# Optimization experiments

Hardware: AMD Instinct MI355X
Metric: run time of the kernel (lower is better)

Reference implementation:

```python
import jax, jax.numpy as jnp
import numpy as np

B, H, S, DK, DV = 2, 16, 2048, 128, 128


def setup_inputs() -> dict:
    key = jax.random.key(0)
    kq, kk, kv = jax.random.split(key, 3)
    query = jax.random.normal(kq, (B, H, S, DK), dtype=jnp.float32)
    k_ = jax.random.normal(kk, (B, H, S, DK), dtype=jnp.float32)
    value = jax.random.normal(kv, (B, H, S, DV), dtype=jnp.float32)
    # causal mask: True = masked out (upper triangle above diagonal)
    causal = ~jnp.tril(jnp.ones((S, S), dtype=bool))
    mask = jnp.broadcast_to(causal[None, None, :, :], (B, 1, S, S))
    return {"query": query, "key": k_, "value": value, "mask": mask}


def reference(query, key, value, mask):
    d_k = query.shape[-1]
    # scores: (B, H, Sq, Sk)
    scores = jnp.einsum("bhqd,bhkd->bhqk", query, key) / jnp.sqrt(jnp.float32(d_k))
    scores = jnp.where(mask, -jnp.inf, scores)
    attention_weights = jax.nn.softmax(scores, axis=-1)
    # dropout p=0.0 (eval) -> identity
    output = jnp.einsum("bhqk,bhkv->bhqv", attention_weights, value)
    return (output, attention_weights)
```

## Files before the change

kernel.cpp:

```cpp
#include <hip/hip_runtime.h>
#include <hip/hip_bf16.h>


typedef __attribute__((ext_vector_type(4))) float  f32x4;
typedef __attribute__((ext_vector_type(8))) short  short8;
typedef __attribute__((ext_vector_type(4))) short  short4v;

#define S_LEN 2048
#define DKK   128
#define QBLK  64
#define KBLK  64
#define NBH   32

__device__ __forceinline__ short f2bf(float f) {
    return __builtin_bit_cast(short, __float2bfloat16(f));
}

__device__ __forceinline__ void g2l16(const void* g, void* l) {
    __builtin_amdgcn_global_load_lds(
        (const __attribute__((address_space(1))) unsigned int*)g,
        (__attribute__((address_space(3))) unsigned int*)l, 16, 0, 0);
}


__global__ __launch_bounds__(256) void conv_k(const float* __restrict__ K,
                                              short* __restrict__ Kb) {
    const int NCH = NBH * S_LEN * (DKK / 8);
    for (int g = blockIdx.x * 256 + threadIdx.x; g < NCH; g += gridDim.x * 256) {
        const int row = g >> 4;
        const int c   = g & 15;
        const float* p = K + (size_t)row * DKK + c * 8;
        f32x4 a = *(const f32x4*)p;
        f32x4 b = *(const f32x4*)(p + 4);
        short8 r;
        #pragma unroll
        for (int j = 0; j < 4; ++j) {
            r[j]     = f2bf(a[j]);
            r[4 + j] = f2bf(b[j]);
        }
        *(short8*)(Kb + (size_t)row * DKK + (size_t)(c ^ (row & 7)) * 8) = r;
    }
}

__global__ __launch_bounds__(256) void conv_vt(const float* __restrict__ V,
                                               short* __restrict__ VT) {
    __shared__ short tile[64][130];
    const int bh = blockIdx.x >> 5;
    const int kt = blockIdx.x & 31;
    const float* Vb = V + ((size_t)bh * S_LEN + kt * 64) * DKK;
    const int t  = threadIdx.x;
    const int k8 = t >> 5, d0 = (t & 31) * 4;
    #pragma unroll
    for (int it = 0; it < 8; ++it) {
        int k = it * 8 + k8;
        f32x4 v = *(const f32x4*)(Vb + (size_t)k * DKK + d0);
        #pragma unroll
        for (int j = 0; j < 4; ++j) tile[k][d0 + j] = f2bf(v[j]);
    }
    __syncthreads();
    const int d = t >> 1, half = t & 1;
    short* outb = VT + (size_t)bh * DKK * S_LEN + (size_t)d * S_LEN + kt * 64;
    #pragma unroll
    for (int cc = 0; cc < 4; ++cc) {
        short8 r;
        #pragma unroll
        for (int j = 0; j < 8; ++j) r[j] = tile[half * 32 + cc * 8 + j][d];
        int cp = (half * 4 + cc) ^ (d & 7);
        *(short8*)(outb + cp * 8) = r;
    }
}


__global__ __launch_bounds__(256) void attn_main(
    const float* __restrict__ Qf, const short* __restrict__ Kb,
    const short* __restrict__ VT, float* __restrict__ O,
    float* __restrict__ W)
{
    __shared__ __align__(16) short kT[2][KBLK * DKK];
    __shared__ __align__(16) short vtT[2][DKK * KBLK];
    __shared__ __align__(16) short pT[4][16 * KBLK];

    const int tid  = threadIdx.x;
    const int lane = tid & 63;
    const int w    = tid >> 6;
    const int lg   = lane >> 4;
    const int lr   = lane & 15;
    const int s7   = lr & 7;

    const int bh = (blockIdx.x & 7) * 4 + ((blockIdx.x >> 3) & 3);
    const int qt = 31 - (blockIdx.x >> 5);
    const int q0 = qt * QBLK;
    const int qbase = q0 + w * 16;
    const int kend  = q0 + QBLK;
    const int ntk   = qt + 1;
    const int qg    = qbase + lr;

    const short* Kbh = Kb + (size_t)bh * S_LEN * DKK;
    const short* VTb = VT + (size_t)bh * DKK * S_LEN;
    float* Ob = O + (size_t)bh * S_LEN * DKK;
    float* Wb = W + (size_t)bh * S_LEN * S_LEN;

    const float QSCALE = 0.08838834764831845f * 1.4426950408889634f;
    short8 qf[4];
    {
        const float* qp = Qf + ((size_t)bh * S_LEN + qg) * DKK + lg * 8;
        #pragma unroll
        for (int ds = 0; ds < 4; ++ds) {
            f32x4 a = *(const f32x4*)(qp + ds * 32);
            f32x4 b = *(const f32x4*)(qp + ds * 32 + 4);
            short8 r;
            #pragma unroll
            for (int jj = 0; jj < 4; ++jj) {
                r[jj]     = f2bf(a[jj] * QSCALE);
                r[4 + jj] = f2bf(b[jj] * QSCALE);
            }
            qf[ds] = r;
        }
    }

    auto stage_k = [&](int buf, int kt_) {
        const char* gk = (const char*)(Kbh + (size_t)kt_ * KBLK * DKK);
        char* lk = (char*)kT[buf];
        #pragma unroll
        for (int i = 0; i < 4; ++i)
            g2l16(gk + i * 4096 + tid * 16, lk + i * 4096 + w * 1024);
    };
    auto stage_v = [&](int buf, int kt_) {
        const char* gv = (const char*)VTb + (size_t)kt_ * (KBLK * 2);
        char* lv = (char*)vtT[buf];
        #pragma unroll
        for (int i = 0; i < 4; ++i) {
            const int L = i * 4096 + tid * 16;
            g2l16(gv + (size_t)(L >> 7) * (S_LEN * 2) + (L & 127),
                  lv + i * 4096 + w * 1024);
        }
    };

    auto k_frag = [&](const char* kBc, int t, int ds) -> short8 {
        const int off = ((16 * t + lr) * 256 + ds * 64 + lg * 16) ^ (s7 << 4);
        return *(const short8*)(kBc + off);
    };

    float lsum = 0.f;
    int cur = 0;
    stage_k(0, 0);
    for (int kt_ = 0; kt_ < ntk; ++kt_) {
        __syncthreads();
        if (kt_ + 1 < ntk) stage_k(cur ^ 1, kt_ + 1);
        const int k0 = kt_ * KBLK;
        const char* kBc = (const char*)kT[cur];
        #pragma unroll
        for (int t = 0; t < 4; ++t) {
            f32x4 d = {0.f, 0.f, 0.f, 0.f};
            __builtin_amdgcn_s_setprio(1);
            #pragma unroll
            for (int ds = 0; ds < 4; ++ds)
                d = __builtin_amdgcn_mfma_f32_16x16x32_bf16(
                        k_frag(kBc, t, ds), qf[ds], d, 0, 0, 0);
            __builtin_amdgcn_s_setprio(0);
            const int kb = k0 + 16 * t + lg * 4;
            #pragma unroll
            for (int r = 0; r < 4; ++r)
                lsum += (kb + r <= qg) ? exp2f(d[r]) : 0.f;
        }
        cur ^= 1;
    }
    lsum += __shfl_xor(lsum, 16);
    lsum += __shfl_xor(lsum, 32);
    const float invl = 1.0f / lsum;

    f32x4 acc[8];
    #pragma unroll
    for (int ii = 0; ii < 8; ++ii) acc[ii] = (f32x4){0.f, 0.f, 0.f, 0.f};

    __syncthreads();
    cur = 0;
    stage_k(0, 0);
    stage_v(0, 0);
    for (int kt_ = 0; kt_ < ntk; ++kt_) {
        __syncthreads();
        if (kt_ + 1 < ntk) { stage_k(cur ^ 1, kt_ + 1); stage_v(cur ^ 1, kt_ + 1); }
        const int k0 = kt_ * KBLK;
        const char* kBc = (const char*)kT[cur];
        const char* vBc = (const char*)vtT[cur];
        char* pBc = (char*)pT[w];

        #pragma unroll
        for (int t = 0; t < 4; ++t) {
            f32x4 d = {0.f, 0.f, 0.f, 0.f};
            __builtin_amdgcn_s_setprio(1);
            #pragma unroll
            for (int ds = 0; ds < 4; ++ds)
                d = __builtin_amdgcn_mfma_f32_16x16x32_bf16(
                        k_frag(kBc, t, ds), qf[ds], d, 0, 0, 0);
            __builtin_amdgcn_s_setprio(0);
            const int kb = k0 + 16 * t + lg * 4;
            f32x4 pv;
            short4v pb;
            #pragma unroll
            for (int r = 0; r < 4; ++r) {
                const float p = (kb + r <= qg) ? exp2f(d[r]) * invl : 0.f;
                pv[r] = p;
                pb[r] = f2bf(p);
            }
            *(f32x4*)(Wb + (size_t)qg * S_LEN + kb) = pv;
            const int poff = lr * 128 + (((16 * t + lg * 4) * 2) ^ (s7 << 4));
            *(short4v*)(pBc + poff) = pb;
        }
        #pragma unroll
        for (int h = 0; h < 2; ++h) {
            const int poff = lr * 128 + ((h * 64 + lg * 16) ^ (s7 << 4));
            short8 pa = *(const short8*)(pBc + poff);
            __builtin_amdgcn_s_setprio(1);
            #pragma unroll
            for (int nt = 0; nt < 8; ++nt) {
                const int voff = (nt * 16 + lr) * 128 + ((h * 64 + lg * 16) ^ (s7 << 4));
                short8 vf = *(const short8*)(vBc + voff);
                acc[nt] = __builtin_amdgcn_mfma_f32_16x16x32_bf16(pa, vf, acc[nt], 0, 0, 0);
            }
            __builtin_amdgcn_s_setprio(0);
        }
        cur ^= 1;
    }

    #pragma unroll
    for (int nt = 0; nt < 8; ++nt)
        #pragma unroll
        for (int r = 0; r < 4; ++r)
            Ob[(size_t)(qbase + lg * 4 + r) * DKK + nt * 16 + lr] = acc[nt][r];

    const int zc = S_LEN - kend;
    if (zc > 0) {
        const int yo = tid >> 2;
        const int xo = tid & 3;
        float* wrow = Wb + (size_t)(q0 + yo) * S_LEN + kend;
        const f32x4 z = {0.f, 0.f, 0.f, 0.f};
        for (int c = xo * 4; c < zc; c += 16)
            *(f32x4*)(wrow + c) = z;
    }
}

extern "C" void kernel_launch(void* const* d_in, const int* in_sizes, int n_in,
                              void* d_out, int out_size, void* d_ws, size_t ws_size,
                              hipStream_t stream) {
    const float* Q = (const float*)d_in[0];
    const float* K = (const float*)d_in[1];
    const float* V = (const float*)d_in[2];
    float* O = (float*)d_out;
    float* W = (float*)d_out + (size_t)NBH * S_LEN * DKK;

    const size_t TEN = (size_t)NBH * S_LEN * DKK;
    short* Kb  = (short*)d_ws;
    short* VTw = Kb + TEN;

    conv_k <<<2048, 256, 0, stream>>>(K, Kb);
    conv_vt<<<1024, 256, 0, stream>>>(V, VTw);
    attn_main<<<1024, 256, 0, stream>>>(Q, Kb, VTw, O, W);
}
```

Before: 231.4 us.

## Split row-sum pass across waves by key tile, reading K directly from global

The first (normalizer) pass now gives each wave a strided subset of key tiles. Every wave computes scores for all 64 query rows from K fragments loaded straight from global memory, with no LDS staging and no per-tile barriers. Partial row sums are reduced through a small shared array, and the first K/V tile for the second pass is prefetched before pass one starts. Launch bounds now request two blocks per CU. This removes per-tile synchronization and the serial LDS loop in pass one, at the cost of much higher register use (Q fragments for four row groups plus 16 K fragments) and uncoalesced global K reads.

Result: slower. 243.5 us (+5.2%).

```diff
diff --git a/kernel.cpp b/kernel.cpp
--- a/kernel.cpp
+++ b/kernel.cpp
@@ -71,7 +71,7 @@
 }
 
 
-__global__ __launch_bounds__(256) void attn_main(
+__global__ __launch_bounds__(256, 2) void attn_main(
     const float* __restrict__ Qf, const short* __restrict__ Kb,
     const short* __restrict__ VT, float* __restrict__ O,
     float* __restrict__ W)
@@ -79,6 +79,7 @@
     __shared__ __align__(16) short kT[2][KBLK * DKK];
     __shared__ __align__(16) short vtT[2][DKK * KBLK];
     __shared__ __align__(16) short pT[4][16 * KBLK];
+    __shared__ float lsum_lds[4][4][16];
 
     const int tid  = threadIdx.x;
     const int lane = tid & 63;
@@ -101,22 +102,19 @@
     float* Wb = W + (size_t)bh * S_LEN * S_LEN;
 
     const float QSCALE = 0.08838834764831845f * 1.4426950408889634f;
-    short8 qf[4];
-    {
-        const float* qp = Qf + ((size_t)bh * S_LEN + qg) * DKK + lg * 8;
-        #pragma unroll
-        for (int ds = 0; ds < 4; ++ds) {
-            f32x4 a = *(const f32x4*)(qp + ds * 32);
-            f32x4 b = *(const f32x4*)(qp + ds * 32 + 4);
-            short8 r;
-            #pragma unroll
-            for (int jj = 0; jj < 4; ++jj) {
-                r[jj]     = f2bf(a[jj] * QSCALE);
-                r[4 + jj] = f2bf(b[jj] * QSCALE);
-            }
-            qf[ds] = r;
-        }
-    }
+
+    auto load_qfrag = [&](int row, int ds) -> short8 {
+        const float* qp = Qf + ((size_t)bh * S_LEN + row) * DKK + lg * 8 + ds * 32;
+        f32x4 a = *(const f32x4*)(qp);
+        f32x4 b = *(const f32x4*)(qp + 4);
+        short8 r;
+        #pragma unroll
+        for (int jj = 0; jj < 4; ++jj) {
+            r[jj]     = f2bf(a[jj] * QSCALE);
+            r[4 + jj] = f2bf(b[jj] * QSCALE);
+        }
+        return r;
+    };
 
     auto stage_k = [&](int buf, int kt_) {
         const char* gk = (const char*)(Kbh + (size_t)kt_ * KBLK * DKK);
@@ -141,42 +139,75 @@
         return *(const short8*)(kBc + off);
     };
 
-    float lsum = 0.f;
-    int cur = 0;
     stage_k(0, 0);
-    for (int kt_ = 0; kt_ < ntk; ++kt_) {
-        __syncthreads();
-        if (kt_ + 1 < ntk) stage_k(cur ^ 1, kt_ + 1);
+    stage_v(0, 0);
+
+    short8 qf[4][4];
+    #pragma unroll
+    for (int g = 0; g < 4; ++g)
+        #pragma unroll
+        for (int ds = 0; ds < 4; ++ds)
+            qf[g][ds] = load_qfrag(q0 + g * 16 + lr, ds);
+
+    float lsg[4] = {0.f, 0.f, 0.f, 0.f};
+    for (int kt_ = w; kt_ < ntk; kt_ += 4) {
         const int k0 = kt_ * KBLK;
-        const char* kBc = (const char*)kT[cur];
+        short8 kr[4][4];
+        #pragma unroll
+        for (int t = 0; t < 4; ++t)
+            #pragma unroll
+            for (int ds = 0; ds < 4; ++ds)
+                kr[t][ds] = *(const short8*)(
+                    Kbh + (size_t)(k0 + 16 * t + lr) * DKK + ((ds * 4 + lg) ^ s7) * 8);
         #pragma unroll
         for (int t = 0; t < 4; ++t) {
-            f32x4 d = {0.f, 0.f, 0.f, 0.f};
+            f32x4 d0 = {0.f, 0.f, 0.f, 0.f};
+            f32x4 d1 = {0.f, 0.f, 0.f, 0.f};
+            f32x4 d2 = {0.f, 0.f, 0.f, 0.f};
+            f32x4 d3 = {0.f, 0.f, 0.f, 0.f};
             __builtin_amdgcn_s_setprio(1);
             #pragma unroll
-            for (int ds = 0; ds < 4; ++ds)
-                d = __builtin_amdgcn_mfma_f32_16x16x32_bf16(
-                        k_frag(kBc, t, ds), qf[ds], d, 0, 0, 0);
+            for (int ds = 0; ds < 4; ++ds) {
+                const short8 kf = kr[t][ds];
+                d0 = __builtin_amdgcn_mfma_f32_16x16x32_bf16(kf, qf[0][ds], d0, 0, 0, 0);
+                d1 = __builtin_amdgcn_mfma_f32_16x16x32_bf16(kf, qf[1][ds], d1, 0, 0, 0);
+                d2 = __builtin_amdgcn_mfma_f32_16x16x32_bf16(kf, qf[2][ds], d2, 0, 0, 0);
+                d3 = __builtin_amdgcn_mfma_f32_16x16x32_bf16(kf, qf[3][ds], d3, 0, 0, 0);
+            }
             __builtin_amdgcn_s_setprio(0);
             const int kb = k0 + 16 * t + lg * 4;
             #pragma unroll
-            for (int r = 0; r < 4; ++r)
-                lsum += (kb + r <= qg) ? exp2f(d[r]) : 0.f;
-        }
-        cur ^= 1;
-    }
-    lsum += __shfl_xor(lsum, 16);
-    lsum += __shfl_xor(lsum, 32);
-    const float invl = 1.0f / lsum;
+            for (int r = 0; r < 4; ++r) {
+                lsg[0] += (kb + r <= q0 + lr)      ? exp2f(d0[r]) : 0.f;
+                lsg[1] += (kb + r <= q0 + 16 + lr) ? exp2f(d1[r]) : 0.f;
+                lsg[2] += (kb + r <= q0 + 32 + lr) ? exp2f(d2[r]) : 0.f;
+                lsg[3] += (kb + r <= q0 + 48 + lr) ? exp2f(d3[r]) : 0.f;
+            }
+        }
+    }
+    #pragma unroll
+    for (int g = 0; g < 4; ++g) {
+        lsg[g] += __shfl_xor(lsg[g], 16);
+        lsg[g] += __shfl_xor(lsg[g], 32);
+    }
+    if (lane < 16) {
+        #pragma unroll
+        for (int g = 0; g < 4; ++g) lsum_lds[w][g][lane] = lsg[g];
+    }
+    __syncthreads();
+    const float invl = 1.0f / (lsum_lds[0][w][lr] + lsum_lds[1][w][lr] +
+                               lsum_lds[2][w][lr] + lsum_lds[3][w][lr]);
+
+    short8 qfw[4];
+    #pragma unroll
+    for (int ds = 0; ds < 4; ++ds)
+        qfw[ds] = load_qfrag(qg, ds);
 
     f32x4 acc[8];
     #pragma unroll
     for (int ii = 0; ii < 8; ++ii) acc[ii] = (f32x4){0.f, 0.f, 0.f, 0.f};
 
-    __syncthreads();
-    cur = 0;
-    stage_k(0, 0);
-    stage_v(0, 0);
+    int cur = 0;
     for (int kt_ = 0; kt_ < ntk; ++kt_) {
         __syncthreads();
         if (kt_ + 1 < ntk) { stage_k(cur ^ 1, kt_ + 1); stage_v(cur ^ 1, kt_ + 1); }
@@ -192,7 +223,7 @@
             #pragma unroll
             for (int ds = 0; ds < 4; ++ds)
                 d = __builtin_amdgcn_mfma_f32_16x16x32_bf16(
-                        k_frag(kBc, t, ds), qf[ds], d, 0, 0, 0);
+                        k_frag(kBc, t, ds), qfw[ds], d, 0, 0, 0);
             __builtin_amdgcn_s_setprio(0);
             const int kb = k0 + 16 * t + lg * 4;
             f32x4 pv;
```
